# Performance work log

Hardware: AMD Instinct MI355X
Metric: run time of the kernel (lower is better)

Reference implementation:

```python
import jax, jax.numpy as jnp
import numpy as np

NB, D, H, DH, DHID = 12, 512, 8, 64, 1024  # n_blocks, d_model, n_heads, d_head, d_hidden
B, S = 2, 2048
EPS = 1e-5


def _ln(x, g, b):
    m = jnp.mean(x, axis=-1, keepdims=True)
    v = jnp.mean(jnp.square(x - m), axis=-1, keepdims=True)
    return (x - m) / jnp.sqrt(v + EPS) * g + b


def setup_inputs() -> dict:
    key = jax.random.key(0)
    ks = jax.random.split(key, 8)
    s = 0.02
    f32 = jnp.float32
    return {
        "X": jax.random.normal(ks[0], (B, S, D), f32),
        "qkv_w": jax.random.normal(ks[1], (NB, D, 3 * D), f32) * s,
        "qkv_b": jnp.zeros((NB, 3 * D), f32),
        "fc_w": jax.random.normal(ks[2], (NB, D, D), f32) * s,
        "fc_b": jnp.zeros((NB, D), f32),
        "ln1_g": jnp.ones((NB, D), f32),
        "ln1_b": jnp.zeros((NB, D), f32),
        "w1": jax.random.normal(ks[3], (NB, D, DHID), f32) * s,
        "b1": jnp.zeros((NB, DHID), f32),
        "w2": jax.random.normal(ks[4], (NB, DHID, D), f32) * s,
        "b2": jnp.zeros((NB, D), f32),
        "ln2_g": jnp.ones((NB, D), f32),
        "ln2_b": jnp.zeros((NB, D), f32),
    }


def reference(X, qkv_w, qkv_b, fc_w, fc_b, ln1_g, ln1_b, w1, b1, w2, b2, ln2_g, ln2_b):
    scale = 1.0 / np.sqrt(D)  # NOTE: original scales by 1/sqrt(d_model), not 1/sqrt(d_head)

    def body(x, p):
        qw, qb, fw, fb, g1, be1, w1_, bb1, w2_, bb2, g2, be2 = p
        b, s, _ = x.shape
        # qkv -> [b, h, s, 3*dh]; split per-head AFTER head reshape (as in chunk(dim=-1))
        ctx = (x @ qw + qb).reshape(b, s, H, 3 * DH).transpose(0, 2, 1, 3)
        q, k, v = jnp.split(ctx, 3, axis=-1)  # each [b, h, s, dh]
        attn = jax.nn.softmax(jnp.einsum('bhqd,bhkd->bhqk', q, k) * scale, axis=-1)
        o = jnp.einsum('bhqk,bhkd->bhqd', attn, v).transpose(0, 2, 1, 3).reshape(b, s, D)
        x = x + (o @ fw + fb)                      # residual + attn out proj (dropout=0)
        h = jax.nn.relu(_ln(x, g1, be1) @ w1_ + bb1)
        x = x + (h @ w2_ + bb2)                    # residual + MLP
        return _ln(x, g2, be2), None

    out, _ = jax.lax.scan(
        body, X,
        (qkv_w, qkv_b, fc_w, fc_b, ln1_g, ln1_b, w1, b1, w2, b2, ln2_g, ln2_b))
    return out
```

## Files before the change

### kernel.cpp

```cpp
#include <hip/hip_runtime.h>

typedef unsigned short ushort_t;
typedef __attribute__((ext_vector_type(8))) short bf16x8;
typedef __attribute__((ext_vector_type(4))) float f32x4;
typedef __attribute__((ext_vector_type(4))) unsigned short us4;

#define DEV __device__ __forceinline__

DEV ushort_t f2b(float f) {
    union { float f; unsigned u; } x; x.f = f;
    unsigned r = (x.u + 0x7fffu + ((x.u >> 16) & 1u)) >> 16;
    return (ushort_t)r;
}

DEV float b2f(ushort_t u) {
    union { unsigned u; float f; } x; x.u = ((unsigned)u) << 16;
    return x.f;
}

DEV unsigned cvt_pk_bf16(float lo, float hi) {
    unsigned r;
    asm("v_cvt_pk_bf16_f32 %0, %1, %2" : "=v"(r) : "v"(lo), "v"(hi));
    return r;
}

typedef void __attribute__((address_space(1)))* gp1;
typedef void __attribute__((address_space(3)))* sp3;
DEV void gload_lds16(const void* g, void* l) {
    __builtin_amdgcn_global_load_lds((gp1)g, (sp3)l, 16, 0, 0);
}

__global__ __launch_bounds__(256) void transpose_cvt(
    const float* __restrict__ in, ushort_t* __restrict__ out, int K, int N)
{
    __shared__ float tile[32][33];
    const int nb = blockIdx.z;
    const float* src = in + (size_t)nb * K * N;
    ushort_t* dst = out + (size_t)nb * K * N;
    const int n0 = blockIdx.x * 32, k0 = blockIdx.y * 32;
    const int tx = threadIdx.x & 31, ty = threadIdx.x >> 5;
#pragma unroll
    for (int i = 0; i < 32; i += 8)
        tile[ty + i][tx] = src[(size_t)(k0 + ty + i) * N + n0 + tx];
    __syncthreads();
#pragma unroll
    for (int i = 0; i < 32; i += 8)
        dst[(size_t)(n0 + ty + i) * K + k0 + tx] = f2b(tile[tx][ty + i]);
}

__global__ __launch_bounds__(256) void init_x(
    const float* __restrict__ X, float* __restrict__ xf, ushort_t* __restrict__ xb)
{
    const int i = blockIdx.x * 256 + threadIdx.x;
    const float4 v = ((const float4*)X)[i];
    ((float4*)xf)[i] = v;
    us4 o = { f2b(v.x), f2b(v.y), f2b(v.z), f2b(v.w) };
    ((us4*)xb)[i] = o;
}

enum { EPI_QKV = 0, EPI_RELUB = 2 };

template<int EPI>
__global__ __launch_bounds__(256, 2) void gemm64(
    const ushort_t* __restrict__ A, const ushort_t* __restrict__ Wt,
    const float* __restrict__ bias, ushort_t* __restrict__ Cb,
    ushort_t* __restrict__ Oq, ushort_t* __restrict__ Ok, ushort_t* __restrict__ Ov,
    int M, int N, int K, float qs)
{
    __shared__ __align__(16) ushort_t lA[2][64 * 64];
    __shared__ __align__(16) ushort_t lB[2][128 * 64];
    const int nbm = M >> 6;
    const int bm = blockIdx.x % nbm;
    const int bn = blockIdx.x / nbm;
    const int tid = threadIdx.x, lane = tid & 63, w = tid >> 6;
    const int l15 = lane & 15, l4 = lane >> 4;

    f32x4 acc[4][2];
#pragma unroll
    for (int i = 0; i < 4; i++)
#pragma unroll
        for (int j = 0; j < 2; j++) { f32x4 z = {0.f, 0.f, 0.f, 0.f}; acc[i][j] = z; }

    const int srow = tid >> 3;
    const int sch = tid & 7;
    const int swch = sch ^ (srow & 7);
    const ushort_t* Asrc0 = A  + (size_t)(bm * 64 + srow) * K + swch * 8;
    const ushort_t* Asrc1 = A  + (size_t)(bm * 64 + srow + 32) * K + swch * 8;
    const ushort_t* Bsrc0 = Wt + (size_t)(bn * 128 + srow) * K + swch * 8;
    const ushort_t* Bsrc1 = Wt + (size_t)(bn * 128 + srow + 32) * K + swch * 8;
    const ushort_t* Bsrc2 = Wt + (size_t)(bn * 128 + srow + 64) * K + swch * 8;
    const ushort_t* Bsrc3 = Wt + (size_t)(bn * 128 + srow + 96) * K + swch * 8;
    char* lAc = (char*)lA;
    char* lBc = (char*)lB;

#define GE_STAGE(buf, k0) do {                                            \
        gload_lds16(Asrc0 + (k0), lAc + (buf) * 8192  + w * 1024);        \
        gload_lds16(Asrc1 + (k0), lAc + (buf) * 8192  + 4096 + w * 1024); \
        gload_lds16(Bsrc0 + (k0), lBc + (buf) * 16384 + w * 1024);        \
        gload_lds16(Bsrc1 + (k0), lBc + (buf) * 16384 + 4096 + w * 1024); \
        gload_lds16(Bsrc2 + (k0), lBc + (buf) * 16384 + 8192 + w * 1024); \
        gload_lds16(Bsrc3 + (k0), lBc + (buf) * 16384 + 12288 + w * 1024);\
    } while (0)

    GE_STAGE(0, 0);
    __syncthreads();

    const int nIt = K >> 6;
    int cur = 0;
    for (int it = 0; it < nIt; ++it) {
        if (it + 1 < nIt) GE_STAGE(cur ^ 1, (it + 1) * 64);
#pragma unroll
        for (int ks = 0; ks < 2; ks++) {
            bf16x8 af[4], bfr[2];
#pragma unroll
            for (int i = 0; i < 4; i++) {
                const int row = i * 16 + l15;
                af[i] = *(const bf16x8*)(lAc + cur * 8192 + row * 128 +
                                         (((ks * 4 + l4) ^ (row & 7)) << 4));
            }
#pragma unroll
            for (int j = 0; j < 2; j++) {
                const int row = w * 32 + j * 16 + l15;
                bfr[j] = *(const bf16x8*)(lBc + cur * 16384 + row * 128 +
                                          (((ks * 4 + l4) ^ (row & 7)) << 4));
            }
#pragma unroll
            for (int i = 0; i < 4; i++)
#pragma unroll
                for (int j = 0; j < 2; j++)
                    acc[i][j] = __builtin_amdgcn_mfma_f32_16x16x32_bf16(af[i], bfr[j], acc[i][j], 0, 0, 0);
        }
        __syncthreads();
        cur ^= 1;
    }
#undef GE_STAGE

    const int mbase = bm * 64;
    const int nbase = bn * 128 + w * 32;
#pragma unroll
    for (int j = 0; j < 2; j++) {
        const int nf16 = nbase + j * 16;
        const float bv = bias[nf16 + l15];
        if constexpr (EPI == EPI_QKV) {
            const int head = nf16 / 192;
            const int rem = nf16 - head * 192;
            const int part = rem >> 6;
            const int dh = (rem & 63) + l15;
#pragma unroll
            for (int i = 0; i < 4; i++) {
                const int m0 = mbase + i * 16 + l4 * 4;
                const int b = m0 >> 11, s0 = m0 & 2047;
                if (part == 2) {
                    us4 pv;
#pragma unroll
                    for (int r = 0; r < 4; r++) pv[r] = f2b(acc[i][j][r] + bv);
                    *(us4*)(&Ov[((size_t)(b * 8 + head) * 64 + dh) * 2048 + s0]) = pv;
                } else if (part == 0) {
#pragma unroll
                    for (int r = 0; r < 4; r++)
                        Oq[((size_t)(b * 8 + head) * 2048 + s0 + r) * 64 + dh] =
                            f2b((acc[i][j][r] + bv) * qs);
                } else {
#pragma unroll
                    for (int r = 0; r < 4; r++)
                        Ok[((size_t)(b * 8 + head) * 2048 + s0 + r) * 64 + dh] =
                            f2b(acc[i][j][r] + bv);
                }
            }
        } else {
#pragma unroll
            for (int i = 0; i < 4; i++) {
                const int m0 = mbase + i * 16 + l4 * 4;
#pragma unroll
                for (int r = 0; r < 4; r++) {
                    const size_t idx = (size_t)(m0 + r) * N + nf16 + l15;
                    const float v = acc[i][j][r] + bv;
                    Cb[idx] = f2b(v > 0.f ? v : 0.f);
                }
            }
        }
    }
}

__global__ __launch_bounds__(256, 2) void gemm64_splitk(
    const ushort_t* __restrict__ A, const ushort_t* __restrict__ Wt,
    ushort_t* __restrict__ P0, ushort_t* __restrict__ P1, int M, int N, int K)
{
    __shared__ __align__(16) ushort_t lA[2][64 * 64];
    __shared__ __align__(16) ushort_t lB[2][128 * 64];
    const int nbm = M >> 6;
    const int nbn = N >> 7;
    int bid = blockIdx.x;
    const int bm = bid % nbm; bid /= nbm;
    const int bn = bid % nbn;
    const int kh = bid / nbn;
    const int Keff = K >> 1;
    const int kbase = kh * Keff;
    const int tid = threadIdx.x, lane = tid & 63, w = tid >> 6;
    const int l15 = lane & 15, l4 = lane >> 4;

    f32x4 acc[4][2];
#pragma unroll
    for (int i = 0; i < 4; i++)
#pragma unroll
        for (int j = 0; j < 2; j++) { f32x4 z = {0.f, 0.f, 0.f, 0.f}; acc[i][j] = z; }

    const int srow = tid >> 3;
    const int sch = tid & 7;
    const int swch = sch ^ (srow & 7);
    const ushort_t* Asrc0 = A  + (size_t)(bm * 64 + srow) * K + kbase + swch * 8;
    const ushort_t* Asrc1 = A  + (size_t)(bm * 64 + srow + 32) * K + kbase + swch * 8;
    const ushort_t* Bsrc0 = Wt + (size_t)(bn * 128 + srow) * K + kbase + swch * 8;
    const ushort_t* Bsrc1 = Wt + (size_t)(bn * 128 + srow + 32) * K + kbase + swch * 8;
    const ushort_t* Bsrc2 = Wt + (size_t)(bn * 128 + srow + 64) * K + kbase + swch * 8;
    const ushort_t* Bsrc3 = Wt + (size_t)(bn * 128 + srow + 96) * K + kbase + swch * 8;
    char* lAc = (char*)lA;
    char* lBc = (char*)lB;

#define GE_STAGE(buf, k0) do {                                            \
        gload_lds16(Asrc0 + (k0), lAc + (buf) * 8192  + w * 1024);        \
        gload_lds16(Asrc1 + (k0), lAc + (buf) * 8192  + 4096 + w * 1024); \
        gload_lds16(Bsrc0 + (k0), lBc + (buf) * 16384 + w * 1024);        \
        gload_lds16(Bsrc1 + (k0), lBc + (buf) * 16384 + 4096 + w * 1024); \
        gload_lds16(Bsrc2 + (k0), lBc + (buf) * 16384 + 8192 + w * 1024); \
        gload_lds16(Bsrc3 + (k0), lBc + (buf) * 16384 + 12288 + w * 1024);\
    } while (0)

    GE_STAGE(0, 0);
    __syncthreads();

    const int nIt = Keff >> 6;
    int cur = 0;
    for (int it = 0; it < nIt; ++it) {
        if (it + 1 < nIt) GE_STAGE(cur ^ 1, (it + 1) * 64);
#pragma unroll
        for (int ks = 0; ks < 2; ks++) {
            bf16x8 af[4], bfr[2];
#pragma unroll
            for (int i = 0; i < 4; i++) {
                const int row = i * 16 + l15;
                af[i] = *(const bf16x8*)(lAc + cur * 8192 + row * 128 +
                                         (((ks * 4 + l4) ^ (row & 7)) << 4));
            }
#pragma unroll
            for (int j = 0; j < 2; j++) {
                const int row = w * 32 + j * 16 + l15;
                bfr[j] = *(const bf16x8*)(lBc + cur * 16384 + row * 128 +
                                          (((ks * 4 + l4) ^ (row & 7)) << 4));
            }
#pragma unroll
            for (int i = 0; i < 4; i++)
#pragma unroll
                for (int j = 0; j < 2; j++)
                    acc[i][j] = __builtin_amdgcn_mfma_f32_16x16x32_bf16(af[i], bfr[j], acc[i][j], 0, 0, 0);
        }
        __syncthreads();
        cur ^= 1;
    }
#undef GE_STAGE

    ushort_t* out = kh ? P1 : P0;
    const int mbase = bm * 64;
    const int nbase = bn * 128 + w * 32;
#pragma unroll
    for (int j = 0; j < 2; j++) {
        const int nf16 = nbase + j * 16;
#pragma unroll
        for (int i = 0; i < 4; i++) {
            const int m0 = mbase + i * 16 + l4 * 4;
#pragma unroll
            for (int r = 0; r < 4; r++)
                out[(size_t)(m0 + r) * N + nf16 + l15] = f2b(acc[i][j][r]);
        }
    }
}

__global__ __launch_bounds__(256, 4) void flash_attn10(
    const ushort_t* __restrict__ Q, const ushort_t* __restrict__ Kg,
    const ushort_t* __restrict__ Vg, ushort_t* __restrict__ Opart,
    float* __restrict__ lbuf)
{
    __shared__ __align__(16) ushort_t lK[2][64 * 64];
    __shared__ __align__(16) ushort_t lV[2][64 * 64];
    __shared__ __align__(16) ushort_t lP[4][16 * 64];

    const int id = blockIdx.x;
    const int rest = id >> 3;
    const int kvh = rest & 1;
    const int qt = (rest >> 1) & 31;
    const int bh = (id & 7) + ((rest >> 6) << 3);
    const int tid = threadIdx.x, lane = tid & 63, w = tid >> 6;
    const int l15 = lane & 15, l4 = lane >> 4;
    const int qrow0 = qt * 64 + w * 16;

    const ushort_t* Qb = Q + ((size_t)bh * 2048 + qrow0) * 64;
    bf16x8 qf[2];
#pragma unroll
    for (int ks = 0; ks < 2; ks++)
        qf[ks] = *(const bf16x8*)(Qb + l15 * 64 + ks * 32 + l4 * 8);

    const ushort_t* Kbase = Kg + (size_t)bh * 2048 * 64;
    const ushort_t* Vbase = Vg + (size_t)bh * 64 * 2048;

    const f32x4 FZ = { 0.f, 0.f, 0.f, 0.f };
    float l_run = 0.f;
    f32x4 oacc[4];
#pragma unroll
    for (int nd = 0; nd < 4; nd++) oacc[nd] = FZ;

    char* lKc = (char*)lK;
    char* lVc = (char*)lV;
    char* myP = (char*)(lP[w]);

    const int srow8 = lane >> 3;
    const int sch = lane & 7;

#define FA_STAGE(buf, kt) do {                                              \
        const int row0_ = w * 16 + srow8;                                   \
        const int sc0_ = sch ^ (row0_ & 7);                                 \
        gload_lds16(Kbase + (size_t)((kt) * 64 + row0_) * 64 + sc0_ * 8,    \
                    lKc + (buf) * 8192 + w * 2048);                         \
        gload_lds16(Vbase + (size_t)row0_ * 2048 + (kt) * 64 + sc0_ * 8,    \
                    lVc + (buf) * 8192 + w * 2048);                         \
        gload_lds16(Kbase + (size_t)((kt) * 64 + row0_ + 8) * 64 + sc0_ * 8,\
                    lKc + (buf) * 8192 + w * 2048 + 1024);                  \
        gload_lds16(Vbase + (size_t)(row0_ + 8) * 2048 + (kt) * 64 + sc0_ * 8,\
                    lVc + (buf) * 8192 + w * 2048 + 1024);                  \
    } while (0)

#define FA_BODY(CUR, IT) do {                                               \
    if ((IT) < 15) FA_STAGE((CUR) ^ 1, kt0 + (IT) + 1);                     \
    f32x4 sc[4];                                                            \
    __builtin_amdgcn_s_setprio(1);                                          \
    _Pragma("unroll")                                                       \
    for (int nf = 0; nf < 4; nf++) {                                        \
        const int krow = nf * 16 + l15;                                     \
        const bf16x8 kf0 = *(const bf16x8*)(lKc + (CUR) * 8192 + krow * 128 + \
                                            ((l4 ^ (krow & 7)) << 4));      \
        const bf16x8 kf1 = *(const bf16x8*)(lKc + (CUR) * 8192 + krow * 128 + \
                                            (((4 + l4) ^ (krow & 7)) << 4)); \
        sc[nf] = __builtin_amdgcn_mfma_f32_16x16x32_bf16(kf0, qf[0], FZ, 0, 0, 0); \
        sc[nf] = __builtin_amdgcn_mfma_f32_16x16x32_bf16(kf1, qf[1], sc[nf], 0, 0, 0); \
    }                                                                       \
    __builtin_amdgcn_s_setprio(0);                                          \
    {                                                                       \
        float ps0 = 0.f, ps1 = 0.f;                                         \
        _Pragma("unroll")                                                   \
        for (int nf = 0; nf < 4; nf++) {                                    \
            const float p0 = exp2f(sc[nf][0]);                              \
            const float p1 = exp2f(sc[nf][1]);                              \
            const float p2 = exp2f(sc[nf][2]);                              \
            const float p3 = exp2f(sc[nf][3]);                              \
            sc[nf][0] = p0; sc[nf][1] = p1;                                 \
            sc[nf][2] = p2; sc[nf][3] = p3;                                 \
            ps0 += p0 + p2; ps1 += p1 + p3;                                 \
        }                                                                   \
        l_run += ps0 + ps1;                                                 \
    }                                                                       \
    const int hh0 = (l15 >> 3) & 1;                                         \
    {                                                                       \
        char* rp = myP + l15 * 128;                                         \
        const int swz = (l15 & 7) << 4;                                     \
        _Pragma("unroll")                                                   \
        for (int nf = 0; nf < 4; nf++) {                                    \
            const unsigned pw0 = cvt_pk_bf16(sc[nf][0], sc[nf][1]);         \
            const unsigned pw1 = cvt_pk_bf16(sc[nf][2], sc[nf][3]);         \
            const unsigned wA = hh0 ? pw1 : pw0;                            \
            const unsigned wB = hh0 ? pw0 : pw1;                            \
            const int cbase = nf * 32 + l4 * 8;                             \
            *(unsigned*)(rp + ((cbase + hh0 * 4) ^ swz)) = wA;              \
            *(unsigned*)(rp + ((cbase + (1 - hh0) * 4) ^ swz)) = wB;        \
        }                                                                   \
    }                                                                       \
    __asm__ volatile("" ::: "memory");                                     \
    bf16x8 pa[2];                                                           \
    _Pragma("unroll")                                                       \
    for (int ks = 0; ks < 2; ks++)                                          \
        pa[ks] = *(const bf16x8*)(myP + l15 * 128 +                         \
                                  ((ks * 64 + l4 * 16) ^ ((l15 & 7) << 4))); \
    __builtin_amdgcn_s_setprio(1);                                          \
    _Pragma("unroll")                                                       \
    for (int ks = 0; ks < 2; ks++)                                          \
        _Pragma("unroll")                                                   \
        for (int nd = 0; nd < 4; nd++) {                                    \
            const int vrow = nd * 16 + l15;                                 \
            const bf16x8 vf = *(const bf16x8*)(lVc + (CUR) * 8192 + vrow * 128 + \
                                               (((ks * 4 + l4) ^ (vrow & 7)) << 4)); \
            oacc[nd] = __builtin_amdgcn_mfma_f32_16x16x32_bf16(pa[ks], vf, oacc[nd], 0, 0, 0); \
        }                                                                   \
    __builtin_amdgcn_s_setprio(0);                                          \
    __syncthreads();                                                        \
} while (0)

    const int kt0 = kvh * 16;
    FA_STAGE(0, kt0);
    __syncthreads();

    for (int it2 = 0; it2 < 8; ++it2) {
        FA_BODY(0, it2 * 2);
        FA_BODY(1, it2 * 2 + 1);
    }
#undef FA_BODY
#undef FA_STAGE

    l_run += __shfl_xor(l_run, 16);
    l_run += __shfl_xor(l_run, 32);
    ushort_t* Op = Opart + ((size_t)(kvh * 16 + bh) * 2048 + qrow0) * 64;
#pragma unroll
    for (int r = 0; r < 4; r++)
#pragma unroll
        for (int nd = 0; nd < 4; nd++)
            Op[(size_t)(l4 * 4 + r) * 64 + nd * 16 + l15] = f2b(oacc[nd][r]);
    if (lane < 16)
        lbuf[(size_t)(kvh * 16 + bh) * 2048 + qrow0 + lane] = l_run;
}

__global__ __launch_bounds__(256) void combine_attn(
    const ushort_t* __restrict__ Opart, const float* __restrict__ lbuf,
    ushort_t* __restrict__ O)
{
    const int gid = blockIdx.x * 256 + threadIdx.x;
    const int d4 = (gid & 15) * 4;
    const int s = (gid >> 4) & 2047;
    const int bh = gid >> 15;
    const us4 a0 = *(const us4*)(Opart + ((size_t)bh * 2048 + s) * 64 + d4);
    const us4 a1 = *(const us4*)(Opart + ((size_t)(16 + bh) * 2048 + s) * 64 + d4);
    const float l0 = lbuf[(size_t)bh * 2048 + s];
    const float l1 = lbuf[(size_t)(16 + bh) * 2048 + s];
    const float inv = 1.f / (l0 + l1);
    us4 out;
#pragma unroll
    for (int r = 0; r < 4; r++)
        out[r] = f2b((b2f(a0[r]) + b2f(a1[r])) * inv);
    const int row = (bh >> 3) * 2048 + s;
    const int col = (bh & 7) * 64 + d4;
    *(us4*)(&O[(size_t)row * 512 + col]) = out;
}

template<int CN>
__global__ __launch_bounds__(256) void ln_fused(
    const float* __restrict__ Xf, const ushort_t* __restrict__ P0,
    const ushort_t* __restrict__ P1, const float* __restrict__ bias,
    const float* __restrict__ g, const float* __restrict__ beta,
    float* __restrict__ XfOut, ushort_t* __restrict__ Yb, float* __restrict__ Yf)
{
    const int row = blockIdx.x * 4 + (threadIdx.x >> 6);
    const int lane = threadIdx.x & 63;
    const size_t base = (size_t)row * 512;
    float4 x0 = ((const float4*)(Xf + base))[lane];
    float4 x1 = ((const float4*)(Xf + base))[lane + 64];
    const us4 a0 = ((const us4*)(P0 + base))[lane];
    const us4 a1 = ((const us4*)(P0 + base))[lane + 64];
    const us4 c0 = ((const us4*)(P1 + base))[lane];
    const us4 c1 = ((const us4*)(P1 + base))[lane + 64];
    const float4 bb0 = ((const float4*)bias)[lane];
    const float4 bb1 = ((const float4*)bias)[lane + 64];
    x0.x += b2f(a0[0]) + b2f(c0[0]) + bb0.x; x0.y += b2f(a0[1]) + b2f(c0[1]) + bb0.y;
    x0.z += b2f(a0[2]) + b2f(c0[2]) + bb0.z; x0.w += b2f(a0[3]) + b2f(c0[3]) + bb0.w;
    x1.x += b2f(a1[0]) + b2f(c1[0]) + bb1.x; x1.y += b2f(a1[1]) + b2f(c1[1]) + bb1.y;
    x1.z += b2f(a1[2]) + b2f(c1[2]) + bb1.z; x1.w += b2f(a1[3]) + b2f(c1[3]) + bb1.w;

    float s = x0.x + x0.y + x0.z + x0.w + x1.x + x1.y + x1.z + x1.w;
    float s2 = x0.x * x0.x + x0.y * x0.y + x0.z * x0.z + x0.w * x0.w
             + x1.x * x1.x + x1.y * x1.y + x1.z * x1.z + x1.w * x1.w;
#pragma unroll
    for (int m = 1; m < 64; m <<= 1) { s += __shfl_xor(s, m); s2 += __shfl_xor(s2, m); }
    const float mean = s * (1.f / 512.f);
    const float inv = rsqrtf(s2 * (1.f / 512.f) - mean * mean + 1e-5f);
    const float4 g0 = ((const float4*)g)[lane], g1 = ((const float4*)g)[lane + 64];
    const float4 b0 = ((const float4*)beta)[lane], b1 = ((const float4*)beta)[lane + 64];
    float4 y0, y1;
    y0.x = (x0.x - mean) * inv * g0.x + b0.x;
    y0.y = (x0.y - mean) * inv * g0.y + b0.y;
    y0.z = (x0.z - mean) * inv * g0.z + b0.z;
    y0.w = (x0.w - mean) * inv * g0.w + b0.w;
    y1.x = (x1.x - mean) * inv * g1.x + b1.x;
    y1.y = (x1.y - mean) * inv * g1.y + b1.y;
    y1.z = (x1.z - mean) * inv * g1.z + b1.z;
    y1.w = (x1.w - mean) * inv * g1.w + b1.w;
    if constexpr (CN == 0) {
        ((float4*)(XfOut + base))[lane] = x0;
        ((float4*)(XfOut + base))[lane + 64] = x1;
    } else {
        ((float4*)(XfOut + base))[lane] = y0;
        ((float4*)(XfOut + base))[lane + 64] = y1;
        if (Yf) {
            ((float4*)(Yf + base))[lane] = y0;
            ((float4*)(Yf + base))[lane + 64] = y1;
        }
    }
    us4 o0 = { f2b(y0.x), f2b(y0.y), f2b(y0.z), f2b(y0.w) };
    us4 o1 = { f2b(y1.x), f2b(y1.y), f2b(y1.z), f2b(y1.w) };
    ((us4*)(Yb + base))[lane] = o0;
    ((us4*)(Yb + base))[lane + 64] = o1;
}

extern "C" void kernel_launch(void* const* d_in, const int* in_sizes, int n_in,
                              void* d_out, int out_size, void* d_ws, size_t ws_size,
                              hipStream_t stream)
{
    (void)in_sizes; (void)n_in; (void)out_size; (void)ws_size;
    const float* X     = (const float*)d_in[0];
    const float* qkv_w = (const float*)d_in[1];
    const float* qkv_b = (const float*)d_in[2];
    const float* fc_w  = (const float*)d_in[3];
    const float* fc_b  = (const float*)d_in[4];
    const float* ln1_g = (const float*)d_in[5];
    const float* ln1_b = (const float*)d_in[6];
    const float* w1    = (const float*)d_in[7];
    const float* b1    = (const float*)d_in[8];
    const float* w2    = (const float*)d_in[9];
    const float* b2    = (const float*)d_in[10];
    const float* ln2_g = (const float*)d_in[11];
    const float* ln2_b = (const float*)d_in[12];

    char* ws = (char*)d_ws;
    size_t off = 0;
    auto alloc = [&](size_t bytes) -> char* {
        char* p = ws + off;
        off += (bytes + 255) & ~(size_t)255;
        return p;
    };
    ushort_t* qkvw_t = (ushort_t*)alloc(12ull * 1536 * 512 * 2);
    ushort_t* fcw_t  = (ushort_t*)alloc(12ull * 512 * 512 * 2);
    ushort_t* w1_t   = (ushort_t*)alloc(12ull * 512 * 1024 * 2);
    ushort_t* w2_t   = (ushort_t*)alloc(12ull * 1024 * 512 * 2);
    float*    xf     = (float*)   alloc(4096ull * 512 * 4);
    ushort_t* xb     = (ushort_t*)alloc(4096ull * 512 * 2);
    ushort_t* qb     = (ushort_t*)alloc(16ull * 2048 * 64 * 2);
    ushort_t* kb     = (ushort_t*)alloc(16ull * 2048 * 64 * 2);
    ushort_t* vt     = (ushort_t*)alloc(16ull * 64 * 2048 * 2);
    ushort_t* ob     = (ushort_t*)alloc(4096ull * 512 * 2);
    ushort_t* y1     = (ushort_t*)alloc(4096ull * 512 * 2);
    ushort_t* hbuf   = (ushort_t*)alloc(4096ull * 1024 * 2);
    ushort_t* opart  = (ushort_t*)alloc(32ull * 2048 * 64 * 2);
    float*    lbuf   = (float*)   alloc(32ull * 2048 * 4);
    ushort_t* pk0 = qb;
    ushort_t* pk1 = kb;

    transpose_cvt<<<dim3(48, 16, 12), 256, 0, stream>>>(qkv_w, qkvw_t, 512, 1536);
    transpose_cvt<<<dim3(16, 16, 12), 256, 0, stream>>>(fc_w, fcw_t, 512, 512);
    transpose_cvt<<<dim3(32, 16, 12), 256, 0, stream>>>(w1, w1_t, 512, 1024);
    transpose_cvt<<<dim3(16, 32, 12), 256, 0, stream>>>(w2, w2_t, 1024, 512);
    init_x<<<2048, 256, 0, stream>>>(X, xf, xb);

    const float sl2 = (float)(0.044194173824159216 * 1.4426950408889634);
    for (int nb = 0; nb < 12; nb++) {
        gemm64<EPI_QKV><<<64 * 12, 256, 0, stream>>>(
            xb, qkvw_t + (size_t)nb * 1536 * 512, qkv_b + nb * 1536,
            nullptr, qb, kb, vt, 4096, 1536, 512, sl2);
        flash_attn10<<<1024, 256, 0, stream>>>(qb, kb, vt, opart, lbuf);
        combine_attn<<<2048, 256, 0, stream>>>(opart, lbuf, ob);
        gemm64_splitk<<<64 * 4 * 2, 256, 0, stream>>>(
            ob, fcw_t + (size_t)nb * 512 * 512, pk0, pk1, 4096, 512, 512);
        ln_fused<0><<<1024, 256, 0, stream>>>(
            xf, pk0, pk1, fc_b + nb * 512, ln1_g + nb * 512, ln1_b + nb * 512,
            xf, y1, nullptr);
        gemm64<EPI_RELUB><<<64 * 8, 256, 0, stream>>>(
            y1, w1_t + (size_t)nb * 1024 * 512, b1 + nb * 1024,
            hbuf, nullptr, nullptr, nullptr, 4096, 1024, 512, 1.f);
        gemm64_splitk<<<64 * 4 * 2, 256, 0, stream>>>(
            hbuf, w2_t + (size_t)nb * 1024 * 512, pk0, pk1, 4096, 512, 1024);
        ln_fused<1><<<1024, 256, 0, stream>>>(
            xf, pk0, pk1, b2 + nb * 512, ln2_g + nb * 512, ln2_b + nb * 512,
            xf, xb, nb == 11 ? (float*)d_out : nullptr);
    }
}
```

Before: 1.129 ms.

## Drop KV split in flash attention and fuse normalization into its epilogue

```diff
diff --git a/kernel.cpp b/kernel.cpp
--- a/kernel.cpp
+++ b/kernel.cpp
@@ -61,7 +61,7 @@
 enum { EPI_QKV = 0, EPI_RELUB = 2 };
 
 template<int EPI>
-__global__ __launch_bounds__(256, 2) void gemm64(
+__global__ __launch_bounds__(256, 3) void gemm64(
     const ushort_t* __restrict__ A, const ushort_t* __restrict__ Wt,
     const float* __restrict__ bias, ushort_t* __restrict__ Cb,
     ushort_t* __restrict__ Oq, ushort_t* __restrict__ Ok, ushort_t* __restrict__ Ov,
@@ -275,10 +275,9 @@
     }
 }
 
-__global__ __launch_bounds__(256, 4) void flash_attn10(
+__global__ __launch_bounds__(256, 4) void flash_attn13(
     const ushort_t* __restrict__ Q, const ushort_t* __restrict__ Kg,
-    const ushort_t* __restrict__ Vg, ushort_t* __restrict__ Opart,
-    float* __restrict__ lbuf)
+    const ushort_t* __restrict__ Vg, ushort_t* __restrict__ O, int niter)
 {
     __shared__ __align__(16) ushort_t lK[2][64 * 64];
     __shared__ __align__(16) ushort_t lV[2][64 * 64];
@@ -286,9 +285,8 @@
 
     const int id = blockIdx.x;
     const int rest = id >> 3;
-    const int kvh = rest & 1;
-    const int qt = (rest >> 1) & 31;
-    const int bh = (id & 7) + ((rest >> 6) << 3);
+    const int qt = rest & 31;
+    const int bh = (id & 7) + ((rest >> 5) << 3);
     const int tid = threadIdx.x, lane = tid & 63, w = tid >> 6;
     const int l15 = lane & 15, l4 = lane >> 4;
     const int qrow0 = qt * 64 + w * 16;
@@ -328,8 +326,8 @@
                     lVc + (buf) * 8192 + w * 2048 + 1024);                  \
     } while (0)
 
-#define FA_BODY(CUR, IT) do {                                               \
-    if ((IT) < 15) FA_STAGE((CUR) ^ 1, kt0 + (IT) + 1);                     \
+#define FA_BODY(CUR, IT, LIM) do {                                          \
+    if ((IT) < (LIM)) FA_STAGE((CUR) ^ 1, (IT) + 1);                        \
     f32x4 sc[4];                                                            \
     __builtin_amdgcn_s_setprio(1);                                          \
     _Pragma("unroll")                                                       \
@@ -392,49 +390,31 @@
     __syncthreads();                                                        \
 } while (0)
 
-    const int kt0 = kvh * 16;
-    FA_STAGE(0, kt0);
+    FA_STAGE(0, 0);
     __syncthreads();
 
-    for (int it2 = 0; it2 < 8; ++it2) {
-        FA_BODY(0, it2 * 2);
-        FA_BODY(1, it2 * 2 + 1);
+    const int lim = niter * 2 - 1;
+#pragma unroll 1
+    for (int it2 = 0; it2 < niter; ++it2) {
+        FA_BODY(0, it2 * 2, lim);
+        FA_BODY(1, it2 * 2 + 1, lim);
     }
 #undef FA_BODY
 #undef FA_STAGE
 
     l_run += __shfl_xor(l_run, 16);
     l_run += __shfl_xor(l_run, 32);
-    ushort_t* Op = Opart + ((size_t)(kvh * 16 + bh) * 2048 + qrow0) * 64;
-#pragma unroll
-    for (int r = 0; r < 4; r++)
+    const int bq = bh >> 3, hh = bh & 7;
+#pragma unroll
+    for (int r = 0; r < 4; r++) {
+        const float lv = __shfl(l_run, l4 * 4 + r);
+        const float inv = 1.f / lv;
+        const int s = qrow0 + l4 * 4 + r;
 #pragma unroll
         for (int nd = 0; nd < 4; nd++)
-            Op[(size_t)(l4 * 4 + r) * 64 + nd * 16 + l15] = f2b(oacc[nd][r]);
-    if (lane < 16)
-        lbuf[(size_t)(kvh * 16 + bh) * 2048 + qrow0 + lane] = l_run;
-}
-
-__global__ __launch_bounds__(256) void combine_attn(
-    const ushort_t* __restrict__ Opart, const float* __restrict__ lbuf,
-    ushort_t* __restrict__ O)
-{
-    const int gid = blockIdx.x * 256 + threadIdx.x;
-    const int d4 = (gid & 15) * 4;
-    const int s = (gid >> 4) & 2047;
-    const int bh = gid >> 15;
-    const us4 a0 = *(const us4*)(Opart + ((size_t)bh * 2048 + s) * 64 + d4);
-    const us4 a1 = *(const us4*)(Opart + ((size_t)(16 + bh) * 2048 + s) * 64 + d4);
-    const float l0 = lbuf[(size_t)bh * 2048 + s];
-    const float l1 = lbuf[(size_t)(16 + bh) * 2048 + s];
-    const float inv = 1.f / (l0 + l1);
-    us4 out;
-#pragma unroll
-    for (int r = 0; r < 4; r++)
-        out[r] = f2b((b2f(a0[r]) + b2f(a1[r])) * inv);
-    const int row = (bh >> 3) * 2048 + s;
-    const int col = (bh & 7) * 64 + d4;
-    *(us4*)(&O[(size_t)row * 512 + col]) = out;
+            O[((size_t)(bq * 2048 + s)) * 512 + hh * 64 + nd * 16 + l15] =
+                f2b(oacc[nd][r] * inv);
+    }
 }
 
 template<int CN>
@@ -533,8 +513,6 @@
     ushort_t* ob     = (ushort_t*)alloc(4096ull * 512 * 2);
     ushort_t* y1     = (ushort_t*)alloc(4096ull * 512 * 2);
     ushort_t* hbuf   = (ushort_t*)alloc(4096ull * 1024 * 2);
-    ushort_t* opart  = (ushort_t*)alloc(32ull * 2048 * 64 * 2);
-    float*    lbuf   = (float*)   alloc(32ull * 2048 * 4);
     ushort_t* pk0 = qb;
     ushort_t* pk1 = kb;
 
@@ -549,8 +527,7 @@
         gemm64<EPI_QKV><<<64 * 12, 256, 0, stream>>>(
             xb, qkvw_t + (size_t)nb * 1536 * 512, qkv_b + nb * 1536,
             nullptr, qb, kb, vt, 4096, 1536, 512, sl2);
-        flash_attn10<<<1024, 256, 0, stream>>>(qb, kb, vt, opart, lbuf);
-        combine_attn<<<2048, 256, 0, stream>>>(opart, lbuf, ob);
+        flash_attn13<<<512, 256, 0, stream>>>(qb, kb, vt, ob, 16);
         gemm64_splitk<<<64 * 4 * 2, 256, 0, stream>>>(
             ob, fcw_t + (size_t)nb * 512 * 512, pk0, pk1, 4096, 512, 512);
         ln_fused<0><<<1024, 256, 0, stream>>>(
```

After: 1.152 ms. 1.02x slower.
